# Performance work log

Hardware: AMD Instinct MI355X
Metric: run time of the kernel (lower is better)

The kernel has to match this reference:

```python
import jax, jax.numpy as jnp
import numpy as np

B, T, D, H, WIN, G = 2, 2048, 768, 12, 16, 32
HD = D // H            # 64
K = 2 * WIN + 1        # local kernel size = 33


def setup_inputs() -> dict:
    key = jax.random.key(0)
    ks = jax.random.split(key, 5)
    s = 1.0 / np.sqrt(D).astype(np.float32)
    x = jax.random.normal(ks[0], (B, T, D), jnp.float32)
    # first G tokens of every batch are global (matches original's nonzero(global_mask[b]))
    global_mask = jnp.zeros((B, T), jnp.int32).at[:, :G].set(1)
    Wq = jax.random.normal(ks[1], (D, D), jnp.float32) * s
    Wk = jax.random.normal(ks[2], (D, D), jnp.float32) * s
    Wv = jax.random.normal(ks[3], (D, D), jnp.float32) * s
    Wo = jax.random.normal(ks[4], (D, D), jnp.float32) * s
    bq = jnp.zeros((D,), jnp.float32)
    bk = jnp.zeros((D,), jnp.float32)
    bv = jnp.zeros((D,), jnp.float32)
    bo = jnp.zeros((D,), jnp.float32)
    return {"x": x, "global_mask": global_mask, "Wq": Wq, "bq": bq,
            "Wk": Wk, "bk": bk, "Wv": Wv, "bv": bv, "Wo": Wo, "bo": bo}


def reference(x, global_mask, Wq, bq, Wk, bk, Wv, bv, Wo, bo):
    def split_heads(y):
        return y.reshape(B, T, H, HD).transpose(0, 2, 1, 3)  # [B,H,T,HD]

    q = split_heads(x @ Wq + bq)
    k = split_heads(x @ Wk + bk)
    v = split_heads(x @ Wv + bv)

    scale = 1.0 / np.sqrt(HD).astype(np.float32)

    offs = jnp.arange(-WIN, WIN + 1)
    idx = jnp.arange(T)[:, None] + offs[None, :]          # [T,K]
    valid = (idx >= 0) & (idx < T)                        # [T,K]
    idxc = jnp.clip(idx, 0, T - 1)

    k_loc = k[:, :, idxc]                                 # [B,H,T,K,HD]
    s_loc = jnp.einsum('bhtd,bhtkd->bhtk', q, k_loc) * scale
    s_loc = jnp.where(valid, s_loc, -jnp.inf)             # out-of-range excluded from softmax

    # global tokens (same positions for every batch by construction)
    g_idx = jnp.nonzero(global_mask[0], size=G)[0]        # [G]
    k_g = k[:, :, g_idx]                                  # [B,H,G,HD]
    v_g = v[:, :, g_idx]
    s_g = jnp.einsum('bhtd,bhgd->bhtg', q, k_g) * scale   # [B,H,T,G]

    # joint softmax over [local window, global tokens] (globals in window are double-counted,
    # exactly as in the original torch.cat([local_s, g_score]))
    attn = jax.nn.softmax(jnp.concatenate([s_loc, s_g], axis=-1), axis=-1)
    a_loc = jnp.where(valid, attn[..., :K], 0.0)          # [B,H,T,K]
    a_g = attn[..., K:]                                   # [B,H,T,G]

    v_loc = v[:, :, idxc]                                 # [B,H,T,K,HD]
    ctx = (jnp.einsum('bhtk,bhtkd->bhtd', a_loc, v_loc)
           + jnp.einsum('bhtg,bhgd->bhtd', a_g, v_g))     # [B,H,T,HD]

    out = ctx.transpose(0, 2, 1, 3).reshape(B, T, D) @ Wo + bo

    # dense attention map: scatter local band (add; invalid entries are 0),
    # then overwrite global columns (matches original write order)
    rows = jnp.arange(T)[:, None]                         # [T,1]
    full_attn = jnp.zeros((B, H, T, T), jnp.float32)
    full_attn = full_attn.at[:, :, rows, idxc].add(a_loc)
    full_attn = full_attn.at[:, :, :, g_idx].set(a_g)
    return out, full_attn
```

## Files before the change

### kernel.cpp

```cpp
#include <hip/hip_runtime.h>

typedef unsigned short u16;
typedef __attribute__((ext_vector_type(4))) u16 u16x4;
typedef __attribute__((ext_vector_type(8))) u16 u16x8;
typedef __attribute__((ext_vector_type(8))) short bf16x8;
typedef __attribute__((ext_vector_type(4))) float f32x4;

#define BB 2
#define TT 2048
#define DD 768
#define NH 12
#define HDIM 64
#define NQKV 2304
#define MM 4096

__device__ __forceinline__ u16 f2bf(float f) {
  unsigned u = __float_as_uint(f);
  u += 0x7fffu + ((u >> 16) & 1u);
  return (u16)(u >> 16);
}
__device__ __forceinline__ float bf2f(u16 s) {
  return __uint_as_float(((unsigned)s) << 16);
}
__device__ __forceinline__ void async_load16(const void* g, void* l) {
  __builtin_amdgcn_global_load_lds((const __attribute__((address_space(1))) void*)g,
                                   (__attribute__((address_space(3))) void*)l, 16, 0, 0);
}

__global__ __launch_bounds__(256) void fill0(float4* __restrict__ p) {
  p[(size_t)blockIdx.x * 256 + threadIdx.x] = make_float4(0.f, 0.f, 0.f, 0.f);
}

__global__ __launch_bounds__(256) void castx(const float* __restrict__ x, u16* __restrict__ xb) {
  int i = blockIdx.x * 256 + threadIdx.x;
  float4 v = ((const float4*)x)[i];
  u16x4 o = { f2bf(v.x), f2bf(v.y), f2bf(v.z), f2bf(v.w) };
  ((u16x4*)xb)[i] = o;
}

__global__ __launch_bounds__(256) void wprep(const float* __restrict__ Wq, const float* __restrict__ Wk,
                                             const float* __restrict__ Wv, const float* __restrict__ Wo,
                                             u16* __restrict__ wqkvT, u16* __restrict__ woT) {
  __shared__ float tile[32][33];
  int z = blockIdx.z;
  const float* W = (z == 0) ? Wq : (z == 1) ? Wk : (z == 2) ? Wv : Wo;
  u16* dst = (z < 3) ? (wqkvT + (size_t)z * DD * DD) : woT;
  int k0 = blockIdx.x * 32, n0 = blockIdx.y * 32;
  int tx = threadIdx.x, ty = threadIdx.y;
#pragma unroll
  for (int j = 0; j < 4; ++j)
    tile[ty + j * 8][tx] = W[(size_t)(k0 + ty + j * 8) * DD + n0 + tx];
  __syncthreads();
#pragma unroll
  for (int j = 0; j < 4; ++j)
    dst[(size_t)(n0 + ty + j * 8) * DD + k0 + tx] = f2bf(tile[tx][ty + j * 8]);
}

__global__ __launch_bounds__(256) void prep_misc(const int* __restrict__ gm,
                                                 const float* __restrict__ bq, const float* __restrict__ bk,
                                                 const float* __restrict__ bv,
                                                 int* __restrict__ gidx, int* __restrict__ gpos,
                                                 float* __restrict__ biasqkv) {
  int tid = threadIdx.x;
  if (tid < 32) gidx[tid] = 0;
  for (int c = tid; c < TT; c += 256) gpos[c] = -1;
  for (int n = tid; n < NQKV; n += 256)
    biasqkv[n] = (n < 768) ? bq[n] : (n < 1536) ? bk[n - 768] : bv[n - 1536];
  __syncthreads();
  if (tid < 64) {
    int lane = tid;
    int base = 0;
    for (int c0 = 0; c0 < TT; c0 += 64) {
      int mval = gm[c0 + lane];
      unsigned long long bal = __ballot(mval != 0);
      int pre = __popcll(bal & ((1ull << lane) - 1ull));
      if (mval && (base + pre) < 32) { gidx[base + pre] = c0 + lane; gpos[c0 + lane] = base + pre; }
      base += __popcll(bal);
      if (base >= 32) break;
    }
  }
}

template <int BM>
__global__ __launch_bounds__(256) void gemm_bt(const u16* __restrict__ A, const u16* __restrict__ BT,
                                               const float* __restrict__ bias, float* __restrict__ C,
                                               int Ndim, int Kd) {
  constexpr int NJ = (BM == 128) ? 4 : 2;
  constexpr int ACH = BM / 32;
  __shared__ __attribute__((aligned(16))) u16 As[BM * 64];
  __shared__ __attribute__((aligned(16))) u16 Bs[128 * 64];
  const int tid = threadIdx.x;
  const int wave = tid >> 6, lane = tid & 63;
  const int m0 = blockIdx.x * BM, n0 = blockIdx.y * 128;
  const int wm = (BM == 128) ? ((wave & 1) << 6) : 0;
  const int wn = (BM == 128) ? ((wave >> 1) << 6) : (wave << 5);
  const int lr = lane & 15, lk = lane >> 4;
  const int srow_b = lane >> 3;
  const int scol = (lane & 7) * 8;

  f32x4 acc[4][NJ] = {};

  const int kIters = Kd >> 6;
  for (int kt = 0; kt < kIters; ++kt) {
#pragma unroll
    for (int cc = 0; cc < ACH; ++cc) {
      int c = wave * ACH + cc;
      int srow = c * 8 + srow_b;
      async_load16(A + (size_t)(m0 + srow) * Kd + (kt << 6) + scol, (void*)(As + c * 512));
    }
#pragma unroll
    for (int cc = 0; cc < 4; ++cc) {
      int c = wave * 4 + cc;
      int srow = c * 8 + srow_b;
      async_load16(BT + (size_t)(n0 + srow) * Kd + (kt << 6) + scol, (void*)(Bs + c * 512));
    }
    __syncthreads();
#pragma unroll
    for (int kc = 0; kc < 2; ++kc) {
      bf16x8 af[4], bfr[NJ];
#pragma unroll
      for (int i = 0; i < 4; ++i)
        af[i] = *(const bf16x8*)(As + (wm + i * 16 + lr) * 64 + kc * 32 + lk * 8);
#pragma unroll
      for (int j = 0; j < NJ; ++j)
        bfr[j] = *(const bf16x8*)(Bs + (wn + j * 16 + lr) * 64 + kc * 32 + lk * 8);
#pragma unroll
      for (int i = 0; i < 4; ++i)
#pragma unroll
        for (int j = 0; j < NJ; ++j)
          acc[i][j] = __builtin_amdgcn_mfma_f32_16x16x32_bf16(af[i], bfr[j], acc[i][j], 0, 0, 0);
    }
    __syncthreads();
  }

#pragma unroll
  for (int i = 0; i < 4; ++i) {
    const int row = m0 + wm + i * 16 + lk * 4;
#pragma unroll
    for (int j = 0; j < NJ; ++j) {
      const int col = n0 + wn + j * 16 + lr;
      const float bs = bias[col];
#pragma unroll
      for (int r = 0; r < 4; ++r)
        C[(size_t)(row + r) * Ndim + col] = acc[i][j][r] + bs;
    }
  }
}

__global__ __launch_bounds__(256) void attn_kernel(const float* __restrict__ qkv,
                                                   const int* __restrict__ gidx,
                                                   const int* __restrict__ gpos,
                                                   u16* __restrict__ ctxb,
                                                   float* __restrict__ fattn) {
  __shared__ __attribute__((aligned(16))) u16 Kl[96 * 72];
  __shared__ __attribute__((aligned(16))) u16 Kg[32 * 72];
  __shared__ __attribute__((aligned(16))) u16 Vl[96 * 72];
  __shared__ __attribute__((aligned(16))) u16 Vg[32 * 72];
  __shared__ __attribute__((aligned(16))) float probs[64 * 68];
  __shared__ int wgpos[96];
  __shared__ int gidxs[32];

  const int tid = threadIdx.x;
  const int blk = blockIdx.x;
  const int chunk = blk & 31;
  const int h = (blk >> 5) % NH;
  const int b = blk / 384;
  const int t0 = chunk << 6;

  {
    const int r = tid >> 4;
    const int c4 = (tid & 15) << 2;
#pragma unroll
    for (int it = 0; it < 6; ++it) {
      int rr = it * 16 + r;
      int t = t0 - 16 + rr;
      t = t < 0 ? 0 : (t > TT - 1 ? TT - 1 : t);
      const float* src = qkv + (size_t)(b * TT + t) * NQKV + h * HDIM;
      float4 kv = *(const float4*)(src + 768 + c4);
      float4 vv = *(const float4*)(src + 1536 + c4);
      u16x4 kb = { f2bf(kv.x), f2bf(kv.y), f2bf(kv.z), f2bf(kv.w) };
      u16x4 vb = { f2bf(vv.x), f2bf(vv.y), f2bf(vv.z), f2bf(vv.w) };
      *(u16x4*)(Kl + rr * 72 + c4) = kb;
      *(u16x4*)(Vl + rr * 72 + c4) = vb;
    }
#pragma unroll
    for (int it = 0; it < 2; ++it) {
      int rr = it * 16 + r;
      int t = gidx[rr];
      const float* src = qkv + (size_t)(b * TT + t) * NQKV + h * HDIM;
      float4 kv = *(const float4*)(src + 768 + c4);
      float4 vv = *(const float4*)(src + 1536 + c4);
      u16x4 kb = { f2bf(kv.x), f2bf(kv.y), f2bf(kv.z), f2bf(kv.w) };
      u16x4 vb = { f2bf(vv.x), f2bf(vv.y), f2bf(vv.z), f2bf(vv.w) };
      *(u16x4*)(Kg + rr * 72 + c4) = kb;
      *(u16x4*)(Vg + rr * 72 + c4) = vb;
    }
    if (tid < 32) gidxs[tid] = gidx[tid];
    if (tid < 96) {
      int t = t0 - 16 + tid;
      wgpos[tid] = ((unsigned)t < TT) ? gpos[t] : -1;
    }
  }
  __syncthreads();

  const int tl = tid >> 2, sub = tid & 3;
  const int t = t0 + tl;
  const float* qp = qkv + (size_t)(b * TT + t) * NQKV + h * HDIM;
  float4 qr[16];
#pragma unroll
  for (int i = 0; i < 16; ++i) qr[i] = ((const float4*)qp)[i];

  float sc[17];
  float mmax = -__builtin_inff();
#pragma unroll
  for (int i = 0; i < 17; ++i) {
    const int s = sub + (i << 2);
    const u16* kp;
    bool valid;
    if (s < 33) { kp = Kl + (tl + s) * 72; int j = t - 16 + s; valid = (j >= 0) && (j < TT); }
    else if (s < 65) { kp = Kg + (s - 33) * 72; valid = true; }
    else { kp = Kg; valid = false; }
    float d = 0.f;
#pragma unroll
    for (int i2 = 0; i2 < 8; ++i2) {
      u16x8 kv = *(const u16x8*)(kp + i2 * 8);
      float4 qa = qr[i2 * 2], qb = qr[i2 * 2 + 1];
      d += qa.x * bf2f(kv[0]) + qa.y * bf2f(kv[1]) + qa.z * bf2f(kv[2]) + qa.w * bf2f(kv[3]);
      d += qb.x * bf2f(kv[4]) + qb.y * bf2f(kv[5]) + qb.z * bf2f(kv[6]) + qb.w * bf2f(kv[7]);
    }
    sc[i] = valid ? d * 0.125f : -__builtin_inff();
    mmax = fmaxf(mmax, sc[i]);
  }
  mmax = fmaxf(mmax, __shfl_xor(mmax, 1));
  mmax = fmaxf(mmax, __shfl_xor(mmax, 2));
  float sum = 0.f;
#pragma unroll
  for (int i = 0; i < 17; ++i) { sc[i] = __expf(sc[i] - mmax); sum += sc[i]; }
  sum += __shfl_xor(sum, 1);
  sum += __shfl_xor(sum, 2);
  const float inv = 1.0f / sum;
#pragma unroll
  for (int i = 0; i < 17; ++i) {
    const int s = sub + (i << 2);
    sc[i] *= inv;
    if (s < 65) probs[tl * 68 + s] = sc[i];
  }
  __syncthreads();

  float cacc[16];
#pragma unroll
  for (int i = 0; i < 16; ++i) cacc[i] = 0.f;
#pragma unroll 1
  for (int k = 0; k < 65; ++k) {
    const float pv = probs[tl * 68 + k];
    const u16* vp = (k < 33) ? (Vl + (tl + k) * 72) : (Vg + (k - 33) * 72);
    const u16* vq = vp + (sub << 4);
    u16x8 v0 = *(const u16x8*)(vq);
    u16x8 v1 = *(const u16x8*)(vq + 8);
#pragma unroll
    for (int e = 0; e < 8; ++e) { cacc[e] += pv * bf2f(v0[e]); cacc[8 + e] += pv * bf2f(v1[e]); }
  }
  {
    u16x8 cb0, cb1;
#pragma unroll
    for (int e = 0; e < 8; ++e) { cb0[e] = f2bf(cacc[e]); cb1[e] = f2bf(cacc[8 + e]); }
    u16* dst = ctxb + (size_t)(b * TT + t) * DD + h * HDIM + (sub << 4);
    *(u16x8*)dst = cb0;
    *(u16x8*)(dst + 8) = cb1;
  }

  float* frow = fattn + ((size_t)(b * NH + h) * TT + t) * TT;
#pragma unroll
  for (int i = 0; i < 17; ++i) {
    const int s = sub + (i << 2);
    const float p = sc[i];
    if (s < 33) {
      int c = t - 16 + s;
      if ((unsigned)c < TT && wgpos[tl + s] < 0) frow[c] = p;
    } else if (s < 65) {
      frow[gidxs[s - 33]] = p;
    }
  }
}

extern "C" void kernel_launch(void* const* d_in, const int* in_sizes, int n_in,
                              void* d_out, int out_size, void* d_ws, size_t ws_size,
                              hipStream_t stream) {
  const float* x  = (const float*)d_in[0];
  const int* gm   = (const int*)d_in[1];
  const float* Wq = (const float*)d_in[2];
  const float* bq = (const float*)d_in[3];
  const float* Wk = (const float*)d_in[4];
  const float* bk = (const float*)d_in[5];
  const float* Wv = (const float*)d_in[6];
  const float* bv = (const float*)d_in[7];
  const float* Wo = (const float*)d_in[8];
  const float* bo = (const float*)d_in[9];

  float* out = (float*)d_out;
  float* fattn = out + (size_t)BB * TT * DD;

  char* p = (char*)d_ws;
  u16* xb      = (u16*)p;  p += (size_t)MM * DD * 2;
  u16* wqkvT   = (u16*)p;  p += (size_t)NQKV * DD * 2;
  u16* woT     = (u16*)p;  p += (size_t)DD * DD * 2;
  float* biasq = (float*)p; p += (size_t)NQKV * 4;
  int* gidx    = (int*)p;  p += 128;
  int* gpos    = (int*)p;  p += (size_t)TT * 4;
  float* qkv   = (float*)p; p += (size_t)MM * NQKV * 4;
  u16* ctxb    = (u16*)p;  p += (size_t)MM * DD * 2;

  castx<<<MM * DD / 4 / 256, 256, 0, stream>>>(x, xb);
  wprep<<<dim3(24, 24, 4), dim3(32, 8), 0, stream>>>(Wq, Wk, Wv, Wo, wqkvT, woT);
  prep_misc<<<1, 256, 0, stream>>>(gm, bq, bk, bv, gidx, gpos, biasq);
  fill0<<<(size_t)BB * NH * TT * TT / 4 / 256, 256, 0, stream>>>((float4*)fattn);
  gemm_bt<128><<<dim3(MM / 128, NQKV / 128), 256, 0, stream>>>(xb, wqkvT, biasq, qkv, NQKV, DD);
  attn_kernel<<<BB * NH * (TT / 64), 256, 0, stream>>>(qkv, gidx, gpos, ctxb, fattn);
  gemm_bt<64><<<dim3(MM / 64, DD / 128), 256, 0, stream>>>(ctxb, woT, bo, out, DD, DD);
}
```

Before: 562.7 us.

## Fuse dense attention-map zero fill into attention kernel and emit bf16 QKV

Removes the separate fill0 pass over the 400MB dense attention map. Each attention block now writes its own 64 full rows with float4 stores, filling band values from shared probs and zeros elsewhere, then overwrites the global columns after a barrier. The QKV GEMM now writes bf16 instead of fp32, which halves QKV traffic and lets the attention kernel load K, V and Q as bf16 directly. Q is now rounded to bf16, which slightly lowers precision.

```diff
diff --git a/kernel.cpp b/kernel.cpp
--- a/kernel.cpp
+++ b/kernel.cpp
@@ -25,10 +25,6 @@
 __device__ __forceinline__ void async_load16(const void* g, void* l) {
   __builtin_amdgcn_global_load_lds((const __attribute__((address_space(1))) void*)g,
                                    (__attribute__((address_space(3))) void*)l, 16, 0, 0);
-}
-
-__global__ __launch_bounds__(256) void fill0(float4* __restrict__ p) {
-  p[(size_t)blockIdx.x * 256 + threadIdx.x] = make_float4(0.f, 0.f, 0.f, 0.f);
 }
 
 __global__ __launch_bounds__(256) void castx(const float* __restrict__ x, u16* __restrict__ xb) {
@@ -81,9 +77,9 @@
   }
 }
 
-template <int BM>
+template <int BM, bool OUTBF>
 __global__ __launch_bounds__(256) void gemm_bt(const u16* __restrict__ A, const u16* __restrict__ BT,
-                                               const float* __restrict__ bias, float* __restrict__ C,
+                                               const float* __restrict__ bias, void* __restrict__ Cv,
                                                int Ndim, int Kd) {
   constexpr int NJ = (BM == 128) ? 4 : 2;
   constexpr int ACH = BM / 32;
@@ -141,13 +137,16 @@
       const int col = n0 + wn + j * 16 + lr;
       const float bs = bias[col];
 #pragma unroll
-      for (int r = 0; r < 4; ++r)
-        C[(size_t)(row + r) * Ndim + col] = acc[i][j][r] + bs;
-    }
-  }
-}
-
-__global__ __launch_bounds__(256) void attn_kernel(const float* __restrict__ qkv,
+      for (int r = 0; r < 4; ++r) {
+        const float val = acc[i][j][r] + bs;
+        if (OUTBF) ((u16*)Cv)[(size_t)(row + r) * Ndim + col] = f2bf(val);
+        else       ((float*)Cv)[(size_t)(row + r) * Ndim + col] = val;
+      }
+    }
+  }
+}
+
+__global__ __launch_bounds__(256) void attn_kernel(const u16* __restrict__ qb,
                                                    const int* __restrict__ gidx,
                                                    const int* __restrict__ gpos,
                                                    u16* __restrict__ ctxb,
@@ -168,32 +167,22 @@
   const int t0 = chunk << 6;
 
   {
-    const int r = tid >> 4;
-    const int c4 = (tid & 15) << 2;
-#pragma unroll
-    for (int it = 0; it < 6; ++it) {
-      int rr = it * 16 + r;
+    const int r = tid >> 3;
+    const int c8 = (tid & 7) << 3;
+#pragma unroll
+    for (int it = 0; it < 3; ++it) {
+      int rr = it * 32 + r;
       int t = t0 - 16 + rr;
       t = t < 0 ? 0 : (t > TT - 1 ? TT - 1 : t);
-      const float* src = qkv + (size_t)(b * TT + t) * NQKV + h * HDIM;
-      float4 kv = *(const float4*)(src + 768 + c4);
-      float4 vv = *(const float4*)(src + 1536 + c4);
-      u16x4 kb = { f2bf(kv.x), f2bf(kv.y), f2bf(kv.z), f2bf(kv.w) };
-      u16x4 vb = { f2bf(vv.x), f2bf(vv.y), f2bf(vv.z), f2bf(vv.w) };
-      *(u16x4*)(Kl + rr * 72 + c4) = kb;
-      *(u16x4*)(Vl + rr * 72 + c4) = vb;
-    }
-#pragma unroll
-    for (int it = 0; it < 2; ++it) {
-      int rr = it * 16 + r;
-      int t = gidx[rr];
-      const float* src = qkv + (size_t)(b * TT + t) * NQKV + h * HDIM;
-      float4 kv = *(const float4*)(src + 768 + c4);
-      float4 vv = *(const float4*)(src + 1536 + c4);
-      u16x4 kb = { f2bf(kv.x), f2bf(kv.y), f2bf(kv.z), f2bf(kv.w) };
-      u16x4 vb = { f2bf(vv.x), f2bf(vv.y), f2bf(vv.z), f2bf(vv.w) };
-      *(u16x4*)(Kg + rr * 72 + c4) = kb;
-      *(u16x4*)(Vg + rr * 72 + c4) = vb;
+      const u16* src = qb + (size_t)(b * TT + t) * NQKV + h * HDIM + c8;
+      *(u16x8*)(Kl + rr * 72 + c8) = *(const u16x8*)(src + 768);
+      *(u16x8*)(Vl + rr * 72 + c8) = *(const u16x8*)(src + 1536);
+    }
+    {
+      int t = gidx[r];
+      const u16* src = qb + (size_t)(b * TT + t) * NQKV + h * HDIM + c8;
+      *(u16x8*)(Kg + r * 72 + c8) = *(const u16x8*)(src + 768);
+      *(u16x8*)(Vg + r * 72 + c8) = *(const u16x8*)(src + 1536);
     }
     if (tid < 32) gidxs[tid] = gidx[tid];
     if (tid < 96) {
@@ -205,10 +194,14 @@
 
   const int tl = tid >> 2, sub = tid & 3;
   const int t = t0 + tl;
-  const float* qp = qkv + (size_t)(b * TT + t) * NQKV + h * HDIM;
-  float4 qr[16];
-#pragma unroll
-  for (int i = 0; i < 16; ++i) qr[i] = ((const float4*)qp)[i];
+  const u16* qp = qb + (size_t)(b * TT + t) * NQKV + h * HDIM;
+  float qv[64];
+#pragma unroll
+  for (int i = 0; i < 8; ++i) {
+    u16x8 qq = *(const u16x8*)(qp + i * 8);
+#pragma unroll
+    for (int e = 0; e < 8; ++e) qv[i * 8 + e] = bf2f(qq[e]);
+  }
 
   float sc[17];
   float mmax = -__builtin_inff();
@@ -224,9 +217,8 @@
 #pragma unroll
     for (int i2 = 0; i2 < 8; ++i2) {
       u16x8 kv = *(const u16x8*)(kp + i2 * 8);
-      float4 qa = qr[i2 * 2], qb = qr[i2 * 2 + 1];
-      d += qa.x * bf2f(kv[0]) + qa.y * bf2f(kv[1]) + qa.z * bf2f(kv[2]) + qa.w * bf2f(kv[3]);
-      d += qb.x * bf2f(kv[4]) + qb.y * bf2f(kv[5]) + qb.z * bf2f(kv[6]) + qb.w * bf2f(kv[7]);
+#pragma unroll
+      for (int e = 0; e < 8; ++e) d += qv[i2 * 8 + e] * bf2f(kv[e]);
     }
     sc[i] = valid ? d * 0.125f : -__builtin_inff();
     mmax = fmaxf(mmax, sc[i]);
@@ -269,17 +261,34 @@
     *(u16x8*)(dst + 8) = cb1;
   }
 
-  float* frow = fattn + ((size_t)(b * NH + h) * TT + t) * TT;
-#pragma unroll
-  for (int i = 0; i < 17; ++i) {
-    const int s = sub + (i << 2);
-    const float p = sc[i];
-    if (s < 33) {
-      int c = t - 16 + s;
-      if ((unsigned)c < TT && wgpos[tl + s] < 0) frow[c] = p;
-    } else if (s < 65) {
-      frow[gidxs[s - 33]] = p;
-    }
+  float* fbase = fattn + ((size_t)(b * NH + h) * TT + t0) * TT;
+#pragma unroll 1
+  for (int it = 0; it < 128; ++it) {
+    int f = it * 256 + tid;
+    int rl = f >> 9;
+    int c4 = (f & 511) << 2;
+    int trow = t0 + rl;
+    float4 v = make_float4(0.f, 0.f, 0.f, 0.f);
+    int kk = c4 - trow + 16;
+    if (kk >= -3 && kk < 33) {
+      const float* pr = probs + rl * 68;
+      float* vp = &v.x;
+#pragma unroll
+      for (int e = 0; e < 4; ++e) {
+        int k2 = kk + e;
+        if ((unsigned)k2 < 33u) vp[e] = pr[k2];
+      }
+    }
+    *(float4*)(fbase + (size_t)rl * TT + c4) = v;
+  }
+  __syncthreads();
+
+  {
+    int rl = tid >> 2, g0 = (tid & 3) << 3;
+    const float* pr = probs + rl * 68 + 33;
+    float* frow = fbase + (size_t)rl * TT;
+#pragma unroll
+    for (int e = 0; e < 8; ++e) frow[gidxs[g0 + e]] = pr[g0 + e];
   }
 }
 
@@ -307,14 +316,13 @@
   float* biasq = (float*)p; p += (size_t)NQKV * 4;
   int* gidx    = (int*)p;  p += 128;
   int* gpos    = (int*)p;  p += (size_t)TT * 4;
-  float* qkv   = (float*)p; p += (size_t)MM * NQKV * 4;
+  u16* qkvb    = (u16*)p;  p += (size_t)MM * NQKV * 2;
   u16* ctxb    = (u16*)p;  p += (size_t)MM * DD * 2;
 
   castx<<<MM * DD / 4 / 256, 256, 0, stream>>>(x, xb);
   wprep<<<dim3(24, 24, 4), dim3(32, 8), 0, stream>>>(Wq, Wk, Wv, Wo, wqkvT, woT);
   prep_misc<<<1, 256, 0, stream>>>(gm, bq, bk, bv, gidx, gpos, biasq);
-  fill0<<<(size_t)BB * NH * TT * TT / 4 / 256, 256, 0, stream>>>((float4*)fattn);
-  gemm_bt<128><<<dim3(MM / 128, NQKV / 128), 256, 0, stream>>>(xb, wqkvT, biasq, qkv, NQKV, DD);
-  attn_kernel<<<BB * NH * (TT / 64), 256, 0, stream>>>(qkv, gidx, gpos, ctxb, fattn);
-  gemm_bt<64><<<dim3(MM / 64, DD / 128), 256, 0, stream>>>(ctxb, woT, bo, out, DD, DD);
-}
+  gemm_bt<128, true><<<dim3(MM / 128, NQKV / 128), 256, 0, stream>>>(xb, wqkvT, biasq, qkvb, NQKV, DD);
+  attn_kernel<<<BB * NH * (TT / 64), 256, 0, stream>>>(qkvb, gidx, gpos, ctxb, fattn);
+  gemm_bt<64, false><<<dim3(MM / 64, DD / 128), 256, 0, stream>>>(ctxb, woT, bo, out, DD, DD);
+}
```

New measurement: 547.9 us. 1.03x faster.
